# Performance work log

Measured on AMD Instinct MI355X. Metric: run time of the kernel, lower is better.

The kernel has to match this reference:

```python
import jax, jax.numpy as jnp
import numpy as np

N, M, K = 4096, 256, 32
W_EPS = 1e-6


def _spd(key, n, k):
    # well-conditioned SPD precision matrices: A A^T / k + I
    a = jax.random.normal(key, (n, k, k), dtype=jnp.float32)
    return jnp.matmul(a, jnp.swapaxes(a, -1, -2)) / k + jnp.eye(k, dtype=jnp.float32)


def setup_inputs() -> dict:
    key = jax.random.key(0)
    k1, k2, k3, k4 = jax.random.split(key, 4)
    W = jax.random.uniform(k1, (N, M), dtype=jnp.float32)
    mu_s = jax.random.normal(k2, (N, K), dtype=jnp.float32)
    omega_child = _spd(k3, N, K)
    omega_parent = _spd(k4, M, K)
    return {"W": W, "mu_s": mu_s, "omega_child": omega_child, "omega_parent": omega_parent}


def reference(W, mu_s, omega_child, omega_parent):
    # mask out negligible memberships (original skips w < 1e-6)
    wT = W.T                                   # (M, N)
    mask = wT >= W_EPS
    w = jnp.where(mask, wT, 0.0)

    # v_i = inv(omega_child_i) @ mu_s_i  -> batched solve, (N, K)
    v = jnp.linalg.solve(omega_child, mu_s[..., None])[..., 0]

    # transported means: Omega_alpha @ v_i, (M, N, K)
    T = jnp.einsum('mkl,nl->mnk', omega_parent, v)

    Z = w.sum(-1)                              # (M,)
    Zs = jnp.maximum(Z, 1e-30)
    mu_bar = jnp.einsum('mn,mnk->mk', w, T) / Zs[:, None]
    diff = T - mu_bar[:, None, :]              # (M, N, K)
    var = jnp.einsum('mn,mnk->mk', w, diff * diff) / Zs[:, None]
    psi = var.sum(-1)                          # (M,)

    # clusters with fewer than 2 contributing agents get psi = 0
    count = mask.sum(-1)
    return jnp.where(count >= 2, psi, 0.0)
```

## Files before the change

### kernel.cpp

```cpp
#include <hip/hip_runtime.h>

constexpr int N_AG = 4096;
constexpr int M_CL = 256;
constexpr int KD   = 32;
constexpr float WEPS = 1e-6f;

constexpr int PART_STRIDE = 1088;
constexpr int V_OFF  = M_CL * 4 * PART_STRIDE;
constexpr int VT_OFF = V_OFF + N_AG * KD;
constexpr int WT_OFF = VT_OFF + N_AG * KD;

typedef __attribute__((ext_vector_type(8))) short short8;
typedef __attribute__((ext_vector_type(4))) float f32x4;

__device__ __forceinline__ float rlane(float x, int l) {
    return __int_as_float(__builtin_amdgcn_readlane(__float_as_int(x), l));
}

template<int J>
struct GJ {
    static __device__ __forceinline__ void run(float (&col)[32]) {
        const float piv  = rlane(col[J], J);
        const float pinv = 1.0f / piv;
        col[J] *= pinv;
        #pragma unroll
        for (int i = 0; i < 32; ++i) {
            if (i == J) continue;
            const float fi = rlane(col[i], J);
            col[i] = fmaf(-fi, col[J], col[i]);
        }
        GJ<J + 1>::run(col);
    }
};
template<> struct GJ<32> {
    static __device__ __forceinline__ void run(float (&)[32]) {}
};

__global__ __launch_bounds__(256, 1) void solve_kernel(const float* __restrict__ oc,
                                                       const float* __restrict__ mu,
                                                       float* __restrict__ v) {
    const int lane = threadIdx.x & 63;
    const int wid  = threadIdx.x >> 6;
    const int idx  = blockIdx.x * 4 + wid;
    const int c = (lane < 32) ? lane : 32;

    float col[32];
    #pragma unroll
    for (int i = 0; i < 32; ++i) {
        col[i] = (c < 32) ? oc[idx * 1024 + i * 32 + c]
                          : mu[idx * 32 + i];
    }

    GJ<0>::run(col);

    float res = 0.0f;
    #pragma unroll
    for (int i = 0; i < 32; ++i) {
        const float xi = rlane(col[i], 32);
        if (lane == i) res = xi;
    }
    if (lane < 32) v[idx * 32 + lane] = res;
}

__global__ __launch_bounds__(256) void transpose_fused(const float* __restrict__ W,
                                                       const float* __restrict__ v,
                                                       float* __restrict__ Wt,
                                                       float* __restrict__ vT) {
    __shared__ float tb[32][33];
    const int x = threadIdx.x & 31;
    const int y = threadIdx.x >> 5;
    const int bid = blockIdx.x;
    if (bid < 1024) {
        const int n0 = (bid & 127) * 32;
        const int m0 = (bid >> 7) * 32;
        #pragma unroll
        for (int r = 0; r < 4; ++r) {
            const int n = y + 8 * r;
            float w = W[(size_t)(n0 + n) * 256 + m0 + x];
            tb[n][x] = (w >= WEPS) ? w : 0.0f;
        }
        __syncthreads();
        #pragma unroll
        for (int r = 0; r < 4; ++r) {
            const int mm = y + 8 * r;
            Wt[(size_t)(m0 + mm) * 4096 + n0 + x] = tb[x][mm];
        }
    } else {
        const int n0 = (bid - 1024) * 32;
        #pragma unroll
        for (int r = 0; r < 4; ++r) {
            const int n = y + 8 * r;
            tb[n][x] = v[(size_t)(n0 + n) * 32 + x];
        }
        __syncthreads();
        #pragma unroll
        for (int r = 0; r < 4; ++r) {
            const int kk = y + 8 * r;
            vT[(size_t)kk * 4096 + n0 + x] = tb[x][kk];
        }
    }
}

__global__ __launch_bounds__(256, 3) void partial_kernel(const float* __restrict__ Wt,
                                                         const float* __restrict__ vT,
                                                         float* __restrict__ wsout) {
    const int m = blockIdx.x >> 2;
    const int p = blockIdx.x & 3;
    const int t = threadIdx.x;
    const int lane = t & 63;
    const int wv   = t >> 6;

    __shared__ unsigned ubuf[4][2][32 * 36];
    __shared__ float swbuf[1024];
    __shared__ float zred[256];
    __shared__ float s1buf[32];

    const float4 wv4 = reinterpret_cast<const float4*>(Wt + (size_t)m * 4096 + p * 1024)[t];
    float zacc = wv4.x + wv4.y + wv4.z + wv4.w;
    float cacc = (wv4.x >= WEPS ? 1.f : 0.f) + (wv4.y >= WEPS ? 1.f : 0.f)
               + (wv4.z >= WEPS ? 1.f : 0.f) + (wv4.w >= WEPS ? 1.f : 0.f);
    reinterpret_cast<float4*>(swbuf)[t] =
        make_float4(sqrtf(wv4.x), sqrtf(wv4.y), sqrtf(wv4.z), sqrtf(wv4.w));
    if (t < 32) s1buf[t] = 0.0f;
    __syncthreads();

    f32x4 Chh[4], Chl[4];
    #pragma unroll
    for (int q = 0; q < 4; ++q) {
        Chh[q] = (f32x4){0.f, 0.f, 0.f, 0.f};
        Chl[q] = (f32x4){0.f, 0.f, 0.f, 0.f};
    }
    float s1acc[4] = {0.f, 0.f, 0.f, 0.f};

    const int krow = lane >> 3;
    const int nsub = (lane & 7) * 4;

    for (int rnd = 0; rnd < 4; ++rnd) {
        const int nloc0 = wv * 256 + rnd * 64;

        #pragma unroll
        for (int it = 0; it < 8; ++it) {
            const int k  = krow + 8 * (it & 3);
            const int nn = nsub + 32 * (it >> 2);
            const float4 v4 = *reinterpret_cast<const float4*>(
                vT + (size_t)k * 4096 + p * 1024 + nloc0 + nn);
            const float4 s4 = *reinterpret_cast<const float4*>(&swbuf[nloc0 + nn]);
            const float ux = v4.x * s4.x, uy = v4.y * s4.y;
            const float uz = v4.z * s4.z, uw = v4.w * s4.w;
            const unsigned bx = __float_as_uint(ux), by = __float_as_uint(uy);
            const unsigned bz = __float_as_uint(uz), bw = __float_as_uint(uw);
            const unsigned hi01 = __builtin_amdgcn_perm(by, bx, 0x07060302u);
            const unsigned hi23 = __builtin_amdgcn_perm(bw, bz, 0x07060302u);
            const float lx = ux - __uint_as_float(bx & 0xFFFF0000u);
            const float ly = uy - __uint_as_float(by & 0xFFFF0000u);
            const float lz = uz - __uint_as_float(bz & 0xFFFF0000u);
            const float lw = uw - __uint_as_float(bw & 0xFFFF0000u);
            const unsigned lo01 = __builtin_amdgcn_perm(__float_as_uint(ly), __float_as_uint(lx), 0x07060302u);
            const unsigned lo23 = __builtin_amdgcn_perm(__float_as_uint(lw), __float_as_uint(lz), 0x07060302u);
            const int dwi = k * 36 + (nn >> 1);
            *reinterpret_cast<uint2*>(&ubuf[wv][0][dwi]) = make_uint2(hi01, hi23);
            *reinterpret_cast<uint2*>(&ubuf[wv][1][dwi]) = make_uint2(lo01, lo23);
            s1acc[it & 3] += ux * s4.x + uy * s4.y + uz * s4.z + uw * s4.w;
        }

        #pragma unroll
        for (int c2 = 0; c2 < 2; ++c2) {
            const int ndw = (c2 * 32 + (lane >> 4) * 8) >> 1;
            const int r0 = (lane & 15) * 36 + ndw;
            const int r1 = r0 + 16 * 36;
            const short8 h0 = *reinterpret_cast<const short8*>(&ubuf[wv][0][r0]);
            const short8 h1 = *reinterpret_cast<const short8*>(&ubuf[wv][0][r1]);
            const short8 l0 = *reinterpret_cast<const short8*>(&ubuf[wv][1][r0]);
            const short8 l1 = *reinterpret_cast<const short8*>(&ubuf[wv][1][r1]);
            Chh[0] = __builtin_amdgcn_mfma_f32_16x16x32_bf16(h0, h0, Chh[0], 0, 0, 0);
            Chh[1] = __builtin_amdgcn_mfma_f32_16x16x32_bf16(h0, h1, Chh[1], 0, 0, 0);
            Chh[2] = __builtin_amdgcn_mfma_f32_16x16x32_bf16(h1, h0, Chh[2], 0, 0, 0);
            Chh[3] = __builtin_amdgcn_mfma_f32_16x16x32_bf16(h1, h1, Chh[3], 0, 0, 0);
            Chl[0] = __builtin_amdgcn_mfma_f32_16x16x32_bf16(h0, l0, Chl[0], 0, 0, 0);
            Chl[1] = __builtin_amdgcn_mfma_f32_16x16x32_bf16(h0, l1, Chl[1], 0, 0, 0);
            Chl[2] = __builtin_amdgcn_mfma_f32_16x16x32_bf16(h1, l0, Chl[2], 0, 0, 0);
            Chl[3] = __builtin_amdgcn_mfma_f32_16x16x32_bf16(h1, l1, Chl[3], 0, 0, 0);
        }
    }

    #pragma unroll
    for (int j = 0; j < 4; ++j) {
        float r = s1acc[j];
        r += __shfl_xor(r, 1);
        r += __shfl_xor(r, 2);
        r += __shfl_xor(r, 4);
        if ((lane & 7) == 0) atomicAdd(&s1buf[krow + 8 * j], r);
    }
    __syncthreads();

    float* redw = reinterpret_cast<float*>(&ubuf[wv][0][0]);
    #pragma unroll
    for (int q = 0; q < 4; ++q) {
        const int I = q >> 1, J = q & 1;
        #pragma unroll
        for (int r = 0; r < 4; ++r) {
            const int a = I * 16 + (lane >> 4) * 4 + r;
            const int b = J * 16 + (lane & 15);
            redw[a * 32 + b] = Chh[q][r] + Chl[q][r];
        }
    }
    __syncthreads();
    #pragma unroll
    for (int q = 0; q < 4; ++q) {
        const int I = q >> 1, J = q & 1;
        #pragma unroll
        for (int r = 0; r < 4; ++r) {
            const int a = I * 16 + (lane >> 4) * 4 + r;
            const int b = J * 16 + (lane & 15);
            redw[b * 32 + a] += Chl[q][r];
        }
    }
    __syncthreads();

    const size_t base = (size_t)(m * 4 + p) * PART_STRIDE;
    float o0 = 0.f, o1 = 0.f, o2 = 0.f, o3 = 0.f;
    #pragma unroll
    for (int ww = 0; ww < 4; ++ww) {
        const float4 x = *reinterpret_cast<const float4*>(
            &reinterpret_cast<float*>(&ubuf[ww][0][0])[t * 4]);
        o0 += x.x; o1 += x.y; o2 += x.z; o3 += x.w;
    }
    *reinterpret_cast<float4*>(&wsout[base + t * 4]) = make_float4(o0, o1, o2, o3);

    zred[t] = zacc; __syncthreads();
    #pragma unroll
    for (int s = 128; s > 0; s >>= 1) {
        if (t < s) zred[t] += zred[t + s];
        __syncthreads();
    }
    if (t == 0) wsout[base + 1056] = zred[0];
    __syncthreads();
    zred[t] = cacc; __syncthreads();
    #pragma unroll
    for (int s = 128; s > 0; s >>= 1) {
        if (t < s) zred[t] += zred[t + s];
        __syncthreads();
    }
    if (t == 0) wsout[base + 1057] = zred[0];
    if (t < 32) wsout[base + 1024 + t] = s1buf[t];
}

__global__ __launch_bounds__(256) void combine_kernel(const float* __restrict__ op,
                                                      const float* __restrict__ ws,
                                                      float* __restrict__ out) {
    const int m = blockIdx.x;
    const int t = threadIdx.x;

    __shared__ float omg[32 * 33];
    __shared__ float vbar[32];
    __shared__ float red[256];

    #pragma unroll
    for (int i = 0; i < 4; ++i) {
        const int g = t + 256 * i;
        const int r = g >> 5, cc = g & 31;
        omg[r * 33 + cc] = op[(size_t)m * 1024 + g];
    }

    const size_t mb = (size_t)m * 4 * PART_STRIDE;
    float Z = 0.0f, cnt = 0.0f, s1 = 0.0f;
    float s2[4] = {0.f, 0.f, 0.f, 0.f};
    #pragma unroll
    for (int p2 = 0; p2 < 4; ++p2) {
        const size_t bp = mb + (size_t)p2 * PART_STRIDE;
        Z   += ws[bp + 1056];
        cnt += ws[bp + 1057];
        if (t < 32) s1 += ws[bp + 1024 + t];
        const float4 sp = *reinterpret_cast<const float4*>(&ws[bp + t * 4]);
        s2[0] += sp.x; s2[1] += sp.y; s2[2] += sp.z; s2[3] += sp.w;
    }
    const float invZ = 1.0f / fmaxf(Z, 1e-30f);
    if (t < 32) vbar[t] = s1 * invZ;
    __syncthreads();

    const int k  = t >> 3;
    const int l0 = (t & 7) * 4;
    float G[4] = {0.f, 0.f, 0.f, 0.f};
    #pragma unroll
    for (int i = 0; i < 32; ++i) {
        const float ok = omg[i * 33 + k];
        #pragma unroll
        for (int q = 0; q < 4; ++q) G[q] = fmaf(ok, omg[i * 33 + l0 + q], G[q]);
    }

    const float vk = vbar[k];
    float val = 0.0f;
    #pragma unroll
    for (int q = 0; q < 4; ++q)
        val += G[q] * (s2[q] * invZ - vk * vbar[l0 + q]);

    red[t] = val; __syncthreads();
    #pragma unroll
    for (int s = 128; s > 0; s >>= 1) {
        if (t < s) red[t] += red[t + s];
        __syncthreads();
    }
    if (t == 0) out[m] = (cnt >= 1.5f) ? red[0] : 0.0f;
}

extern "C" void kernel_launch(void* const* d_in, const int* in_sizes, int n_in,
                              void* d_out, int out_size, void* d_ws, size_t ws_size,
                              hipStream_t stream) {
    const float* W  = (const float*)d_in[0];
    const float* mu = (const float*)d_in[1];
    const float* oc = (const float*)d_in[2];
    const float* op = (const float*)d_in[3];
    float* out = (float*)d_out;
    float* ws  = (float*)d_ws;

    solve_kernel<<<1024, 256, 0, stream>>>(oc, mu, ws + V_OFF);
    transpose_fused<<<1152, 256, 0, stream>>>(W, ws + V_OFF, ws + WT_OFF, ws + VT_OFF);
    partial_kernel<<<1024, 256, 0, stream>>>(ws + WT_OFF, ws + VT_OFF, ws);
    combine_kernel<<<256, 256, 0, stream>>>(op, ws, out);
}
```

Before: 115.5 us.

## Fuse solve with transposes, dual-matrix GJ per wave, register-direct MFMA operands

Merges the solve and transpose kernels into one launch. Each wave now solves two systems interleaved for ILP, and v is written straight out transposed through a small shared buffer. The partial kernel builds bf16 hi/lo MFMA operands directly in registers from global loads, dropping the LDS staging round-trip, and occupancy is raised to 4 blocks. This removes a kernel launch and the v round-trip through memory. The cost is higher register pressure in the solve and a larger shared reduction buffer.

```diff
diff --git a/kernel.cpp b/kernel.cpp
--- a/kernel.cpp
+++ b/kernel.cpp
@@ -6,8 +6,7 @@
 constexpr float WEPS = 1e-6f;
 
 constexpr int PART_STRIDE = 1088;
-constexpr int V_OFF  = M_CL * 4 * PART_STRIDE;
-constexpr int VT_OFF = V_OFF + N_AG * KD;
+constexpr int VT_OFF = M_CL * 4 * PART_STRIDE;
 constexpr int WT_OFF = VT_OFF + N_AG * KD;
 
 typedef __attribute__((ext_vector_type(8))) short short8;
@@ -16,67 +15,88 @@
 __device__ __forceinline__ float rlane(float x, int l) {
     return __int_as_float(__builtin_amdgcn_readlane(__float_as_int(x), l));
 }
+__device__ __forceinline__ short8 mk8(unsigned a, unsigned b, unsigned c, unsigned d) {
+    union { unsigned u[4]; short8 s; } x;
+    x.u[0] = a; x.u[1] = b; x.u[2] = c; x.u[3] = d;
+    return x.s;
+}
 
 template<int J>
-struct GJ {
-    static __device__ __forceinline__ void run(float (&col)[32]) {
-        const float piv  = rlane(col[J], J);
-        const float pinv = 1.0f / piv;
-        col[J] *= pinv;
+struct GJ2 {
+    static __device__ __forceinline__ void run(float (&ca)[32], float (&cb)[32]) {
+        const float pa = rlane(ca[J], J);
+        const float pb = rlane(cb[J], J);
+        const float ia = 1.0f / pa;
+        const float ib = 1.0f / pb;
+        ca[J] *= ia;
+        cb[J] *= ib;
         #pragma unroll
         for (int i = 0; i < 32; ++i) {
             if (i == J) continue;
-            const float fi = rlane(col[i], J);
-            col[i] = fmaf(-fi, col[J], col[i]);
-        }
-        GJ<J + 1>::run(col);
+            const float fa = rlane(ca[i], J);
+            const float fb = rlane(cb[i], J);
+            ca[i] = fmaf(-fa, ca[J], ca[i]);
+            cb[i] = fmaf(-fb, cb[J], cb[i]);
+        }
+        GJ2<J + 1>::run(ca, cb);
     }
 };
-template<> struct GJ<32> {
-    static __device__ __forceinline__ void run(float (&)[32]) {}
+template<> struct GJ2<32> {
+    static __device__ __forceinline__ void run(float (&)[32], float (&)[32]) {}
 };
 
-__global__ __launch_bounds__(256, 1) void solve_kernel(const float* __restrict__ oc,
-                                                       const float* __restrict__ mu,
-                                                       float* __restrict__ v) {
-    const int lane = threadIdx.x & 63;
-    const int wid  = threadIdx.x >> 6;
-    const int idx  = blockIdx.x * 4 + wid;
+__global__ __launch_bounds__(256, 1) void solve_transpose_kernel(
+        const float* __restrict__ oc, const float* __restrict__ mu,
+        const float* __restrict__ W,
+        float* __restrict__ vT, float* __restrict__ Wt) {
+    __shared__ float res8[32][8];
+    __shared__ float tb[32][33];
+
+    const int t    = threadIdx.x;
+    const int lane = t & 63;
+    const int wv   = t >> 6;
+    const int idx0 = blockIdx.x * 8;
+    const int ia_  = idx0 + 2 * wv;
+    const int ib_  = ia_ + 1;
     const int c = (lane < 32) ? lane : 32;
 
-    float col[32];
+    float ca[32], cb[32];
     #pragma unroll
     for (int i = 0; i < 32; ++i) {
-        col[i] = (c < 32) ? oc[idx * 1024 + i * 32 + c]
-                          : mu[idx * 32 + i];
-    }
-
-    GJ<0>::run(col);
-
-    float res = 0.0f;
+        ca[i] = (c < 32) ? oc[ia_ * 1024 + i * 32 + c] : mu[ia_ * 32 + i];
+        cb[i] = (c < 32) ? oc[ib_ * 1024 + i * 32 + c] : mu[ib_ * 32 + i];
+    }
+
+    GJ2<0>::run(ca, cb);
+
+    float ra = 0.0f, rb = 0.0f;
     #pragma unroll
     for (int i = 0; i < 32; ++i) {
-        const float xi = rlane(col[i], 32);
-        if (lane == i) res = xi;
-    }
-    if (lane < 32) v[idx * 32 + lane] = res;
-}
-
-__global__ __launch_bounds__(256) void transpose_fused(const float* __restrict__ W,
-                                                       const float* __restrict__ v,
-                                                       float* __restrict__ Wt,
-                                                       float* __restrict__ vT) {
-    __shared__ float tb[32][33];
-    const int x = threadIdx.x & 31;
-    const int y = threadIdx.x >> 5;
-    const int bid = blockIdx.x;
-    if (bid < 1024) {
-        const int n0 = (bid & 127) * 32;
-        const int m0 = (bid >> 7) * 32;
+        const float xa = rlane(ca[i], 32);
+        const float xb = rlane(cb[i], 32);
+        if (lane == i) { ra = xa; rb = xb; }
+    }
+    if (lane < 32) {
+        res8[lane][2 * wv]     = ra;
+        res8[lane][2 * wv + 1] = rb;
+    }
+    __syncthreads();
+    {
+        const int k = t >> 3, j = t & 7;
+        vT[(size_t)k * 4096 + idx0 + j] = res8[k][j];
+    }
+
+    const int x = t & 31, y = t >> 5;
+    #pragma unroll
+    for (int rep = 0; rep < 2; ++rep) {
+        const int tile = blockIdx.x * 2 + rep;
+        const int n0 = (tile & 127) * 32;
+        const int m0 = (tile >> 7) * 32;
+        __syncthreads();
         #pragma unroll
         for (int r = 0; r < 4; ++r) {
             const int n = y + 8 * r;
-            float w = W[(size_t)(n0 + n) * 256 + m0 + x];
+            const float w = W[(size_t)(n0 + n) * 256 + m0 + x];
             tb[n][x] = (w >= WEPS) ? w : 0.0f;
         }
         __syncthreads();
@@ -85,23 +105,10 @@
             const int mm = y + 8 * r;
             Wt[(size_t)(m0 + mm) * 4096 + n0 + x] = tb[x][mm];
         }
-    } else {
-        const int n0 = (bid - 1024) * 32;
-        #pragma unroll
-        for (int r = 0; r < 4; ++r) {
-            const int n = y + 8 * r;
-            tb[n][x] = v[(size_t)(n0 + n) * 32 + x];
-        }
-        __syncthreads();
-        #pragma unroll
-        for (int r = 0; r < 4; ++r) {
-            const int kk = y + 8 * r;
-            vT[(size_t)kk * 4096 + n0 + x] = tb[x][kk];
-        }
-    }
-}
-
-__global__ __launch_bounds__(256, 3) void partial_kernel(const float* __restrict__ Wt,
+    }
+}
+
+__global__ __launch_bounds__(256, 4) void partial_kernel(const float* __restrict__ Wt,
                                                          const float* __restrict__ vT,
                                                          float* __restrict__ wsout) {
     const int m = blockIdx.x >> 2;
@@ -110,98 +117,113 @@
     const int lane = t & 63;
     const int wv   = t >> 6;
 
-    __shared__ unsigned ubuf[4][2][32 * 36];
     __shared__ float swbuf[1024];
-    __shared__ float zred[256];
+    __shared__ float sred[4 * 1024];
+    __shared__ float red[256];
     __shared__ float s1buf[32];
 
     const float4 wv4 = reinterpret_cast<const float4*>(Wt + (size_t)m * 4096 + p * 1024)[t];
-    float zacc = wv4.x + wv4.y + wv4.z + wv4.w;
-    float cacc = (wv4.x >= WEPS ? 1.f : 0.f) + (wv4.y >= WEPS ? 1.f : 0.f)
-               + (wv4.z >= WEPS ? 1.f : 0.f) + (wv4.w >= WEPS ? 1.f : 0.f);
+    const float zacc = wv4.x + wv4.y + wv4.z + wv4.w;
+    const float cacc = (wv4.x >= WEPS ? 1.f : 0.f) + (wv4.y >= WEPS ? 1.f : 0.f)
+                     + (wv4.z >= WEPS ? 1.f : 0.f) + (wv4.w >= WEPS ? 1.f : 0.f);
     reinterpret_cast<float4*>(swbuf)[t] =
         make_float4(sqrtf(wv4.x), sqrtf(wv4.y), sqrtf(wv4.z), sqrtf(wv4.w));
     if (t < 32) s1buf[t] = 0.0f;
     __syncthreads();
 
+    const int a = lane & 15;
+    const int g = lane >> 4;
+    const int nl = wv * 256 + g * 8;
+
+    const float4* pa4 = reinterpret_cast<const float4*>(vT + (size_t)a * 4096 + p * 1024 + nl);
+    const float4* pb4 = reinterpret_cast<const float4*>(vT + (size_t)(a + 16) * 4096 + p * 1024 + nl);
+
     f32x4 Chh[4], Chl[4];
     #pragma unroll
     for (int q = 0; q < 4; ++q) {
         Chh[q] = (f32x4){0.f, 0.f, 0.f, 0.f};
         Chl[q] = (f32x4){0.f, 0.f, 0.f, 0.f};
     }
-    float s1acc[4] = {0.f, 0.f, 0.f, 0.f};
-
-    const int krow = lane >> 3;
-    const int nsub = (lane & 7) * 4;
-
-    for (int rnd = 0; rnd < 4; ++rnd) {
-        const int nloc0 = wv * 256 + rnd * 64;
-
-        #pragma unroll
-        for (int it = 0; it < 8; ++it) {
-            const int k  = krow + 8 * (it & 3);
-            const int nn = nsub + 32 * (it >> 2);
-            const float4 v4 = *reinterpret_cast<const float4*>(
-                vT + (size_t)k * 4096 + p * 1024 + nloc0 + nn);
-            const float4 s4 = *reinterpret_cast<const float4*>(&swbuf[nloc0 + nn]);
-            const float ux = v4.x * s4.x, uy = v4.y * s4.y;
-            const float uz = v4.z * s4.z, uw = v4.w * s4.w;
-            const unsigned bx = __float_as_uint(ux), by = __float_as_uint(uy);
-            const unsigned bz = __float_as_uint(uz), bw = __float_as_uint(uw);
-            const unsigned hi01 = __builtin_amdgcn_perm(by, bx, 0x07060302u);
-            const unsigned hi23 = __builtin_amdgcn_perm(bw, bz, 0x07060302u);
-            const float lx = ux - __uint_as_float(bx & 0xFFFF0000u);
-            const float ly = uy - __uint_as_float(by & 0xFFFF0000u);
-            const float lz = uz - __uint_as_float(bz & 0xFFFF0000u);
-            const float lw = uw - __uint_as_float(bw & 0xFFFF0000u);
-            const unsigned lo01 = __builtin_amdgcn_perm(__float_as_uint(ly), __float_as_uint(lx), 0x07060302u);
-            const unsigned lo23 = __builtin_amdgcn_perm(__float_as_uint(lw), __float_as_uint(lz), 0x07060302u);
-            const int dwi = k * 36 + (nn >> 1);
-            *reinterpret_cast<uint2*>(&ubuf[wv][0][dwi]) = make_uint2(hi01, hi23);
-            *reinterpret_cast<uint2*>(&ubuf[wv][1][dwi]) = make_uint2(lo01, lo23);
-            s1acc[it & 3] += ux * s4.x + uy * s4.y + uz * s4.z + uw * s4.w;
-        }
-
-        #pragma unroll
-        for (int c2 = 0; c2 < 2; ++c2) {
-            const int ndw = (c2 * 32 + (lane >> 4) * 8) >> 1;
-            const int r0 = (lane & 15) * 36 + ndw;
-            const int r1 = r0 + 16 * 36;
-            const short8 h0 = *reinterpret_cast<const short8*>(&ubuf[wv][0][r0]);
-            const short8 h1 = *reinterpret_cast<const short8*>(&ubuf[wv][0][r1]);
-            const short8 l0 = *reinterpret_cast<const short8*>(&ubuf[wv][1][r0]);
-            const short8 l1 = *reinterpret_cast<const short8*>(&ubuf[wv][1][r1]);
-            Chh[0] = __builtin_amdgcn_mfma_f32_16x16x32_bf16(h0, h0, Chh[0], 0, 0, 0);
-            Chh[1] = __builtin_amdgcn_mfma_f32_16x16x32_bf16(h0, h1, Chh[1], 0, 0, 0);
-            Chh[2] = __builtin_amdgcn_mfma_f32_16x16x32_bf16(h1, h0, Chh[2], 0, 0, 0);
-            Chh[3] = __builtin_amdgcn_mfma_f32_16x16x32_bf16(h1, h1, Chh[3], 0, 0, 0);
-            Chl[0] = __builtin_amdgcn_mfma_f32_16x16x32_bf16(h0, l0, Chl[0], 0, 0, 0);
-            Chl[1] = __builtin_amdgcn_mfma_f32_16x16x32_bf16(h0, l1, Chl[1], 0, 0, 0);
-            Chl[2] = __builtin_amdgcn_mfma_f32_16x16x32_bf16(h1, l0, Chl[2], 0, 0, 0);
-            Chl[3] = __builtin_amdgcn_mfma_f32_16x16x32_bf16(h1, l1, Chl[3], 0, 0, 0);
-        }
-    }
-
-    #pragma unroll
-    for (int j = 0; j < 4; ++j) {
-        float r = s1acc[j];
-        r += __shfl_xor(r, 1);
-        r += __shfl_xor(r, 2);
-        r += __shfl_xor(r, 4);
-        if ((lane & 7) == 0) atomicAdd(&s1buf[krow + 8 * j], r);
-    }
-    __syncthreads();
-
-    float* redw = reinterpret_cast<float*>(&ubuf[wv][0][0]);
+    float s1a = 0.0f, s1b = 0.0f;
+
+    #pragma unroll 2
+    for (int ch = 0; ch < 8; ++ch) {
+        const float4 va0 = pa4[ch * 8];
+        const float4 va1 = pa4[ch * 8 + 1];
+        const float4 vb0 = pb4[ch * 8];
+        const float4 vb1 = pb4[ch * 8 + 1];
+        const float4 s0  = *reinterpret_cast<const float4*>(&swbuf[nl + ch * 32]);
+        const float4 s1v = *reinterpret_cast<const float4*>(&swbuf[nl + ch * 32 + 4]);
+
+        const float ua0 = va0.x * s0.x,  ua1 = va0.y * s0.y;
+        const float ua2 = va0.z * s0.z,  ua3 = va0.w * s0.w;
+        const float ua4 = va1.x * s1v.x, ua5 = va1.y * s1v.y;
+        const float ua6 = va1.z * s1v.z, ua7 = va1.w * s1v.w;
+        const float ub0 = vb0.x * s0.x,  ub1 = vb0.y * s0.y;
+        const float ub2 = vb0.z * s0.z,  ub3 = vb0.w * s0.w;
+        const float ub4 = vb1.x * s1v.x, ub5 = vb1.y * s1v.y;
+        const float ub6 = vb1.z * s1v.z, ub7 = vb1.w * s1v.w;
+
+        s1a += s0.x*ua0 + s0.y*ua1 + s0.z*ua2 + s0.w*ua3
+             + s1v.x*ua4 + s1v.y*ua5 + s1v.z*ua6 + s1v.w*ua7;
+        s1b += s0.x*ub0 + s0.y*ub1 + s0.z*ub2 + s0.w*ub3
+             + s1v.x*ub4 + s1v.y*ub5 + s1v.z*ub6 + s1v.w*ub7;
+
+        #define BITS(u) __float_as_uint(u)
+        #define LO(u)  ((u) - __uint_as_float(BITS(u) & 0xFFFF0000u))
+        const short8 h0 = mk8(
+            __builtin_amdgcn_perm(BITS(ua1), BITS(ua0), 0x07060302u),
+            __builtin_amdgcn_perm(BITS(ua3), BITS(ua2), 0x07060302u),
+            __builtin_amdgcn_perm(BITS(ua5), BITS(ua4), 0x07060302u),
+            __builtin_amdgcn_perm(BITS(ua7), BITS(ua6), 0x07060302u));
+        const short8 h1 = mk8(
+            __builtin_amdgcn_perm(BITS(ub1), BITS(ub0), 0x07060302u),
+            __builtin_amdgcn_perm(BITS(ub3), BITS(ub2), 0x07060302u),
+            __builtin_amdgcn_perm(BITS(ub5), BITS(ub4), 0x07060302u),
+            __builtin_amdgcn_perm(BITS(ub7), BITS(ub6), 0x07060302u));
+        const float la0 = LO(ua0), la1 = LO(ua1), la2 = LO(ua2), la3 = LO(ua3);
+        const float la4 = LO(ua4), la5 = LO(ua5), la6 = LO(ua6), la7 = LO(ua7);
+        const float lb0 = LO(ub0), lb1 = LO(ub1), lb2 = LO(ub2), lb3 = LO(ub3);
+        const float lb4 = LO(ub4), lb5 = LO(ub5), lb6 = LO(ub6), lb7 = LO(ub7);
+        const short8 l0 = mk8(
+            __builtin_amdgcn_perm(BITS(la1), BITS(la0), 0x07060302u),
+            __builtin_amdgcn_perm(BITS(la3), BITS(la2), 0x07060302u),
+            __builtin_amdgcn_perm(BITS(la5), BITS(la4), 0x07060302u),
+            __builtin_amdgcn_perm(BITS(la7), BITS(la6), 0x07060302u));
+        const short8 l1 = mk8(
+            __builtin_amdgcn_perm(BITS(lb1), BITS(lb0), 0x07060302u),
+            __builtin_amdgcn_perm(BITS(lb3), BITS(lb2), 0x07060302u),
+            __builtin_amdgcn_perm(BITS(lb5), BITS(lb4), 0x07060302u),
+            __builtin_amdgcn_perm(BITS(lb7), BITS(lb6), 0x07060302u));
+        #undef BITS
+        #undef LO
+
+        Chh[0] = __builtin_amdgcn_mfma_f32_16x16x32_bf16(h0, h0, Chh[0], 0, 0, 0);
+        Chh[1] = __builtin_amdgcn_mfma_f32_16x16x32_bf16(h0, h1, Chh[1], 0, 0, 0);
+        Chh[2] = __builtin_amdgcn_mfma_f32_16x16x32_bf16(h1, h0, Chh[2], 0, 0, 0);
+        Chh[3] = __builtin_amdgcn_mfma_f32_16x16x32_bf16(h1, h1, Chh[3], 0, 0, 0);
+        Chl[0] = __builtin_amdgcn_mfma_f32_16x16x32_bf16(h0, l0, Chl[0], 0, 0, 0);
+        Chl[1] = __builtin_amdgcn_mfma_f32_16x16x32_bf16(h0, l1, Chl[1], 0, 0, 0);
+        Chl[2] = __builtin_amdgcn_mfma_f32_16x16x32_bf16(h1, l0, Chl[2], 0, 0, 0);
+        Chl[3] = __builtin_amdgcn_mfma_f32_16x16x32_bf16(h1, l1, Chl[3], 0, 0, 0);
+    }
+
+    s1a += __shfl_xor(s1a, 16); s1a += __shfl_xor(s1a, 32);
+    s1b += __shfl_xor(s1b, 16); s1b += __shfl_xor(s1b, 32);
+    if (lane < 16) {
+        atomicAdd(&s1buf[a], s1a);
+        atomicAdd(&s1buf[a + 16], s1b);
+    }
+
+    float* rw = &sred[wv * 1024];
     #pragma unroll
     for (int q = 0; q < 4; ++q) {
         const int I = q >> 1, J = q & 1;
         #pragma unroll
         for (int r = 0; r < 4; ++r) {
-            const int a = I * 16 + (lane >> 4) * 4 + r;
-            const int b = J * 16 + (lane & 15);
-            redw[a * 32 + b] = Chh[q][r] + Chl[q][r];
+            const int ar = I * 16 + (lane >> 4) * 4 + r;
+            const int br = J * 16 + (lane & 15);
+            rw[ar * 32 + br] = Chh[q][r] + Chl[q][r];
         }
     }
     __syncthreads();
@@ -210,9 +232,9 @@
         const int I = q >> 1, J = q & 1;
         #pragma unroll
         for (int r = 0; r < 4; ++r) {
-            const int a = I * 16 + (lane >> 4) * 4 + r;
-            const int b = J * 16 + (lane & 15);
-            redw[b * 32 + a] += Chl[q][r];
+            const int ar = I * 16 + (lane >> 4) * 4 + r;
+            const int br = J * 16 + (lane & 15);
+            rw[br * 32 + ar] += Chl[q][r];
         }
     }
     __syncthreads();
@@ -221,27 +243,26 @@
     float o0 = 0.f, o1 = 0.f, o2 = 0.f, o3 = 0.f;
     #pragma unroll
     for (int ww = 0; ww < 4; ++ww) {
-        const float4 x = *reinterpret_cast<const float4*>(
-            &reinterpret_cast<float*>(&ubuf[ww][0][0])[t * 4]);
+        const float4 x = *reinterpret_cast<const float4*>(&sred[ww * 1024 + t * 4]);
         o0 += x.x; o1 += x.y; o2 += x.z; o3 += x.w;
     }
     *reinterpret_cast<float4*>(&wsout[base + t * 4]) = make_float4(o0, o1, o2, o3);
 
-    zred[t] = zacc; __syncthreads();
+    red[t] = zacc; __syncthreads();
     #pragma unroll
     for (int s = 128; s > 0; s >>= 1) {
-        if (t < s) zred[t] += zred[t + s];
-        __syncthreads();
-    }
-    if (t == 0) wsout[base + 1056] = zred[0];
-    __syncthreads();
-    zred[t] = cacc; __syncthreads();
+        if (t < s) red[t] += red[t + s];
+        __syncthreads();
+    }
+    if (t == 0) wsout[base + 1056] = red[0];
+    __syncthreads();
+    red[t] = cacc; __syncthreads();
     #pragma unroll
     for (int s = 128; s > 0; s >>= 1) {
-        if (t < s) zred[t] += zred[t + s];
-        __syncthreads();
-    }
-    if (t == 0) wsout[base + 1057] = zred[0];
+        if (t < s) red[t] += red[t + s];
+        __syncthreads();
+    }
+    if (t == 0) wsout[base + 1057] = red[0];
     if (t < 32) wsout[base + 1024 + t] = s1buf[t];
 }
 
@@ -313,8 +334,7 @@
     float* out = (float*)d_out;
     float* ws  = (float*)d_ws;
 
-    solve_kernel<<<1024, 256, 0, stream>>>(oc, mu, ws + V_OFF);
-    transpose_fused<<<1152, 256, 0, stream>>>(W, ws + V_OFF, ws + WT_OFF, ws + VT_OFF);
+    solve_transpose_kernel<<<512, 256, 0, stream>>>(oc, mu, W, ws + VT_OFF, ws + WT_OFF);
     partial_kernel<<<1024, 256, 0, stream>>>(ws + WT_OFF, ws + VT_OFF, ws);
     combine_kernel<<<256, 256, 0, stream>>>(op, ws, out);
 }
```

Result: no change. 115.6 us (+0.1%).
